# Kernel optimization log

Hardware: AMD Instinct MI355X
Metric: run time of the kernel (lower is better)

Reference implementation:

```python
import jax, jax.numpy as jnp
import numpy as np

B, DV, W, H = 128, 2048, 14, 14
S = W * H            # 196 spatial positions
DQ = 2048            # question vector dim
DA = 1200            # attention dim_v == dim_q == dim_mm (MLB elementwise fusion)
G = 4                # nb_glimpses
DH = 2048            # fusion dim_h (total); per-glimpse = DH // G
NANS = 3000


def setup_inputs() -> dict:
    key = jax.random.key(0)
    ks = jax.random.split(key, 16)
    s = 0.02
    return {
        "input_v": jax.random.normal(ks[0], (B, DV, W, H), jnp.float32),
        "x_q_vec": jax.random.normal(ks[1], (B, DQ), jnp.float32),
        # conv_v_att: 1x1 conv DV->DA  (expressed as channel matmul)
        "Wv_att": jax.random.normal(ks[2], (DV, DA), jnp.float32) * s,
        "bv_att": jnp.zeros((DA,), jnp.float32),
        # linear_q_att: DQ->DA
        "Wq_att": jax.random.normal(ks[3], (DQ, DA), jnp.float32) * s,
        "bq_att": jnp.zeros((DA,), jnp.float32),
        # conv_att: 1x1 conv DA->G
        "Wa": jax.random.normal(ks[4], (DA, G), jnp.float32) * s,
        "ba": jnp.zeros((G,), jnp.float32),
        # per-glimpse fusion linears DV -> DH//G, stacked over glimpses
        "Wf": jax.random.normal(ks[5], (G, DV, DH // G), jnp.float32) * s,
        "bf": jnp.zeros((G, DH // G), jnp.float32),
        # linear_q_fusion: DQ -> DH
        "Wqf": jax.random.normal(ks[6], (DQ, DH), jnp.float32) * s,
        "bqf": jnp.zeros((DH,), jnp.float32),
        # linear_classif: DH -> NANS
        "Wc": jax.random.normal(ks[7], (DH, NANS), jnp.float32) * s,
        "bc": jnp.zeros((NANS,), jnp.float32),
    }


def reference(input_v, x_q_vec, Wv_att, bv_att, Wq_att, bq_att, Wa, ba,
              Wf, bf, Wqf, bqf, Wc, bc):
    b = input_v.shape[0]
    v_flat = input_v.reshape(b, DV, S)                      # [B, DV, S]

    # --- attention scores ---
    # conv_v_att (1x1) + tanh -> [B, S, DA]
    x_v = jnp.tanh(jnp.einsum('bcs,cd->bsd', v_flat, Wv_att) + bv_att)
    # linear_q_att + tanh -> [B, DA], broadcast over spatial
    x_q = jnp.tanh(x_q_vec @ Wq_att + bq_att)
    # MLB fusion_att: elementwise multiply, then tanh (activation_mm)
    x_att = jnp.tanh(x_v * x_q[:, None, :])                 # [B, S, DA]
    scores = jnp.einsum('bsd,dg->bsg', x_att, Wa) + ba      # [B, S, G]
    att = jax.nn.softmax(scores, axis=1)                    # softmax over spatial

    # --- weighted pooling per glimpse ---
    v_att = jnp.einsum('bsg,bcs->bgc', att, v_flat)         # [B, G, DV]

    # --- fusion of glimpses ---
    xv = jnp.tanh(jnp.einsum('bgc,gch->bgh', v_att, Wf) + bf)  # [B, G, DH/G]
    xv = xv.reshape(b, DH)                                   # concat glimpses
    xq = jnp.tanh(x_q_vec @ Wqf + bqf)                       # [B, DH]
    x = xv * xq                                              # MLB fusion_classif

    # --- classifier ---
    x = jnp.tanh(x)
    return x @ Wc + bc                                       # [B, NANS]
```

## Files before the change

### kernel.cpp

```cpp
#include <hip/hip_runtime.h>
#include <hip/hip_bf16.h>

#define BB   128
#define DV   2048
#define SS   196
#define DQ   2048
#define DA   1200
#define DAP  1280
#define GG   4
#define DH   2048
#define NANS 3000
#define NANSP 3008
#define MROWS (BB*SS)
#define NT   5
#define KSPLIT 8
#define KCHUNK (DV/KSPLIT)
#define NQ   (DAP + DH)

typedef __attribute__((ext_vector_type(8))) short bf16x8;
typedef __attribute__((ext_vector_type(4))) float f32x4;

__device__ __forceinline__ float fast_tanh(float x) {
    float e = __expf(2.0f * x);
    return 1.0f - 2.0f * __builtin_amdgcn_rcpf(e + 1.0f);
}

__device__ __forceinline__ void async_copy16(const void* gsrc, void* ldst) {
    __builtin_amdgcn_global_load_lds(
        (const __attribute__((address_space(1))) void*)gsrc,
        (__attribute__((address_space(3))) void*)ldst, 16, 0, 0);
}

__global__ void pad_misc(const float* __restrict__ bv, const float* __restrict__ Wa,
                         float* __restrict__ bvp, float* __restrict__ wap) {
    int i = blockIdx.x * 256 + threadIdx.x;
    if (i < DAP) bvp[i] = (i < DA) ? bv[i] : 0.f;
    if (i < DAP * GG) {
        int d = i >> 2;
        wap[i] = (d < DA) ? Wa[i] : 0.f;
    }
}

__global__ __launch_bounds__(256) void transpose_v(const float* __restrict__ v,
                                                   __hip_bfloat16* __restrict__ vt) {
    __shared__ float tile[128][65];
    const int b  = blockIdx.z;
    const int c0 = blockIdx.x * 128;
    const int s0 = blockIdx.y * 64;
    const int t  = threadIdx.x;
    const int sl = t & 63;
    const int cr = t >> 6;
    const float* src = v + (size_t)b * DV * SS;
    const int sg = s0 + sl;
    const bool sok = sg < SS;
#pragma unroll
    for (int i = 0; i < 32; ++i) {
        int c = cr + i * 4;
        tile[c][sl] = sok ? src[(size_t)(c0 + c) * SS + sg] : 0.f;
    }
    __syncthreads();
    const int cp = (t & 63) * 2;
#pragma unroll
    for (int i = 0; i < 16; ++i) {
        int s = (t >> 6) + i * 4;
        int sgl = s0 + s;
        if (sgl < SS) {
            __hip_bfloat162 h2;
            h2.x = __float2bfloat16(tile[cp][s]);
            h2.y = __float2bfloat16(tile[cp + 1][s]);
            *(__hip_bfloat162*)(vt + ((size_t)b * SS + sgl) * DV + c0 + cp) = h2;
        }
    }
}

__global__ __launch_bounds__(256) void transpose_w(const float* __restrict__ Wv,
                                                   __hip_bfloat16* __restrict__ wvt) {
    __shared__ float tile[64][65];
    const int d0 = blockIdx.x * 64;
    const int c0 = blockIdx.y * 64;
    const int t  = threadIdx.x;
    const int col  = t & 63;
    const int rowb = t >> 6;
#pragma unroll
    for (int i = 0; i < 16; ++i) {
        int c = rowb + i * 4;
        int d = d0 + col;
        tile[c][col] = (d < DA) ? Wv[(size_t)(c0 + c) * DA + d] : 0.f;
    }
    __syncthreads();
#pragma unroll
    for (int i = 0; i < 16; ++i) {
        int dl = rowb + i * 4;
        wvt[(size_t)(d0 + dl) * DV + c0 + col] = __float2bfloat16(tile[col][dl]);
    }
}

template <int SEL>
__global__ __launch_bounds__(256) void gemm_partial(
    const float* __restrict__ A, int lda,
    const float* __restrict__ Bm, const float* __restrict__ B2,
    float* __restrict__ Cp, int Npad) {
    __shared__ float As[64 * 132];
    __shared__ float Bs[64 * 68];
    const int t     = threadIdx.x;
    const int n0    = blockIdx.x * 64;
    const int kbase = blockIdx.y * KCHUNK;

    const float* Aeff = A;
    const float* Beff;
    int ldb, ncol0, nlim;
    if (SEL == 0) {
        Beff = Bm; ldb = NANS; ncol0 = n0; nlim = NANS;
    } else if (SEL == 1) {
        int gg = n0 >> 9;
        Aeff = A + gg * 2048;
        Beff = Bm + (size_t)gg * 2048 * 512;
        ldb = 512; ncol0 = n0 & 511; nlim = 1 << 30;
    } else {
        if (n0 < DAP) { Beff = Bm; ldb = DA; ncol0 = n0;      nlim = DA; }
        else          { Beff = B2; ldb = DH; ncol0 = n0 - DAP; nlim = 1 << 30; }
    }

    const int tm = (t & 31) * 4;
    const int tn = (t >> 5) * 8;
    float acc[4][8] = {};

    for (int k0 = kbase; k0 < kbase + KCHUNK; k0 += 64) {
        {
            int kk = t & 63, mb = (t >> 6) * 32;
#pragma unroll
            for (int i = 0; i < 32; ++i)
                As[kk * 132 + mb + i] = Aeff[(size_t)(mb + i) * lda + k0 + kk];
        }
        {
            int j = t & 63, kr = t >> 6;
            bool ok = (ncol0 + j) < nlim;
#pragma unroll
            for (int i = 0; i < 16; ++i) {
                int k = kr + i * 4;
                Bs[k * 68 + j] = ok ? Beff[(size_t)(k0 + k) * ldb + ncol0 + j] : 0.f;
            }
        }
        __syncthreads();
#pragma unroll
        for (int kk = 0; kk < 64; ++kk) {
            const float4 av = *(const float4*)(As + kk * 132 + tm);
            const float4 b0 = *(const float4*)(Bs + kk * 68 + tn);
            const float4 b1 = *(const float4*)(Bs + kk * 68 + tn + 4);
            const float am[4] = {av.x, av.y, av.z, av.w};
#pragma unroll
            for (int i = 0; i < 4; ++i) {
                acc[i][0] += am[i] * b0.x; acc[i][1] += am[i] * b0.y;
                acc[i][2] += am[i] * b0.z; acc[i][3] += am[i] * b0.w;
                acc[i][4] += am[i] * b1.x; acc[i][5] += am[i] * b1.y;
                acc[i][6] += am[i] * b1.z; acc[i][7] += am[i] * b1.w;
            }
        }
        __syncthreads();
    }
#pragma unroll
    for (int i = 0; i < 4; ++i) {
        size_t base = ((size_t)blockIdx.y * 128 + tm + i) * Npad + n0 + tn;
        float4 v0 = {acc[i][0], acc[i][1], acc[i][2], acc[i][3]};
        float4 v1 = {acc[i][4], acc[i][5], acc[i][6], acc[i][7]};
        *(float4*)(Cp + base) = v0;
        *(float4*)(Cp + base + 4) = v1;
    }
}

template <int MODE>
__global__ __launch_bounds__(256) void gemm_epilogue(
    const float* __restrict__ Cp, int Npad, int Nreal,
    const float* __restrict__ bias, const float* __restrict__ aux,
    float* __restrict__ out, int ldo) {
    int n = blockIdx.x * 256 + threadIdx.x;
    int m = blockIdx.y;
    if (n >= Npad) return;
    float s = 0.f;
#pragma unroll
    for (int ks = 0; ks < KSPLIT; ++ks)
        s += Cp[((size_t)ks * 128 + m) * Npad + n];
    if (MODE == 0) {
        if (n >= Nreal) return;
        out[(size_t)m * ldo + n] = s + bias[n];
    } else {
        float xv = fast_tanh(s + bias[n]);
        out[(size_t)m * ldo + n] = fast_tanh(xv * aux[(size_t)m * 2048 + n]);
    }
}

__global__ __launch_bounds__(256) void epilogue_q(
    const float* __restrict__ Cp,
    const float* __restrict__ bqa, const float* __restrict__ bqf,
    float* __restrict__ qatt, float* __restrict__ qfus) {
    int n = blockIdx.x * 256 + threadIdx.x;
    int m = blockIdx.y;
    if (n >= NQ) return;
    float s = 0.f;
#pragma unroll
    for (int ks = 0; ks < KSPLIT; ++ks)
        s += Cp[((size_t)ks * 128 + m) * NQ + n];
    if (n < DAP) {
        qatt[(size_t)m * DAP + n] = (n < DA) ? fast_tanh(s + bqa[n]) : 0.f;
    } else {
        int j = n - DAP;
        qfus[(size_t)m * DH + j] = fast_tanh(s + bqf[j]);
    }
}

__global__ __launch_bounds__(512, 2) void big_gemm(
    const __hip_bfloat16* __restrict__ vt,
    const __hip_bfloat16* __restrict__ wt,
    const float* __restrict__ bvp,
    const float* __restrict__ qatt,
    const float* __restrict__ wap,
    float* __restrict__ scores_p) {
    __shared__ __align__(16) char lds[131072];
    __shared__ __align__(16) float wa_s[256 * 4];
    __shared__ float qs[3 * 256];

    const int t    = threadIdx.x;
    const int lane = t & 63;
    const int w    = t >> 6;
    const int wr   = w >> 2;
    const int wc   = w & 3;

    int bid = blockIdx.x;
    int grp = bid / 40, r = bid % 40;
    int mt, nt;
    if (grp < 12) { mt = grp * 8 + (r & 7); nt = r >> 3; }
    else          { mt = 96 + (r & 1);      nt = r >> 1; }
    const int m0 = mt * 256, n0 = nt * 256;
    const int b_lo = m0 / SS;
    const int bs1  = (b_lo + 1) * SS;
    const int bs2  = (b_lo + 2) * SS;

    if (t < 256) *(float4*)(wa_s + t * 4) = *(const float4*)(wap + (n0 + t) * 4);
    {
        int j = t >> 8, c = t & 255;
        int b = b_lo + j;
        qs[t] = (b < BB) ? qatt[(size_t)b * DAP + n0 + c] : 0.f;
        if (t < 256) {
            int b2 = b_lo + 2;
            qs[512 + t] = (b2 < BB) ? qatt[(size_t)b2 * DAP + n0 + t] : 0.f;
        }
    }

    const int srow   = lane >> 3;
    const int schunk = (lane & 7) ^ srow;
    const __hip_bfloat16* aG = vt + (size_t)(m0 + w * 8 + srow) * DV + schunk * 8;
    const __hip_bfloat16* bG = wt + (size_t)(n0 + w * 8 + srow) * DV + schunk * 8;

    auto STAGE = [&](int buf, int kk) {
        char* aL = lds + buf * 65536 + w * 1024;
        char* bL = aL + 32768;
#pragma unroll
        for (int j = 0; j < 4; ++j) {
            async_copy16(aG + (size_t)(j * 64) * DV + kk, aL + j * 8192);
            async_copy16(bG + (size_t)(j * 64) * DV + kk, bL + j * 8192);
        }
    };

    f32x4 acc[8][4];
#pragma unroll
    for (int i = 0; i < 8; ++i)
#pragma unroll
        for (int j = 0; j < 4; ++j) acc[i][j] = (f32x4){0.f, 0.f, 0.f, 0.f};

    STAGE(0, 0);

    for (int kt = 0; kt < 32; ++kt) {
        const int cur = kt & 1;
        __builtin_amdgcn_s_barrier();
        if (kt < 31) {
            STAGE(cur ^ 1, (kt + 1) * 64);
            asm volatile("s_waitcnt vmcnt(8)" ::: "memory");
        } else {
            asm volatile("s_waitcnt vmcnt(0)" ::: "memory");
        }
        __builtin_amdgcn_s_barrier();

        const __hip_bfloat16* As = (const __hip_bfloat16*)(lds + cur * 65536);
        const __hip_bfloat16* Bs = As + 16384;
        bf16x8 a[4], b[4];
#pragma unroll
        for (int ks = 0; ks < 2; ++ks) {
            const int cx = ((ks * 4 + (lane >> 4)) ^ (lane & 7)) * 8;
#pragma unroll
            for (int ni = 0; ni < 4; ++ni)
                b[ni] = *(const bf16x8*)(Bs + (wc * 64 + ni * 16 + (lane & 15)) * 64 + cx);
#pragma unroll
            for (int h = 0; h < 2; ++h) {
#pragma unroll
                for (int q = 0; q < 4; ++q)
                    a[q] = *(const bf16x8*)(As + (wr * 128 + (h * 4 + q) * 16 + (lane & 15)) * 64 + cx);
                __builtin_amdgcn_s_setprio(1);
#pragma unroll
                for (int q = 0; q < 4; ++q)
#pragma unroll
                    for (int ni = 0; ni < 4; ++ni)
                        acc[h * 4 + q][ni] = __builtin_amdgcn_mfma_f32_16x16x32_bf16(
                            a[q], b[ni], acc[h * 4 + q][ni], 0, 0, 0);
                __builtin_amdgcn_s_setprio(0);
            }
        }
    }

    __syncthreads();
    float* sc = (float*)lds;

    const int colb_l = wc * 64 + (lane & 15);
    const int colb_g = n0 + colb_l;
    float bvv[4];
    float4 wv[4];
#pragma unroll
    for (int ni = 0; ni < 4; ++ni) {
        bvv[ni] = bvp[colb_g + ni * 16];
        wv[ni]  = *(const float4*)(wa_s + (colb_l + ni * 16) * 4);
    }
#pragma unroll
    for (int mi = 0; mi < 8; ++mi) {
#pragma unroll
        for (int rr = 0; rr < 4; ++rr) {
            int lrow = wr * 128 + mi * 16 + ((lane >> 4) << 2) + rr;
            int row  = m0 + lrow;
            int qoff = (row >= bs1 ? 256 : 0) + (row >= bs2 ? 256 : 0);
            float p0 = 0.f, p1 = 0.f, p2 = 0.f, p3 = 0.f;
#pragma unroll
            for (int ni = 0; ni < 4; ++ni) {
                float xv = fast_tanh(acc[mi][ni][rr] + bvv[ni]);
                float xa = fast_tanh(xv * qs[qoff + colb_l + ni * 16]);
                p0 += xa * wv[ni].x; p1 += xa * wv[ni].y;
                p2 += xa * wv[ni].z; p3 += xa * wv[ni].w;
            }
#pragma unroll
            for (int mk = 1; mk < 16; mk <<= 1) {
                p0 += __shfl_xor(p0, mk); p1 += __shfl_xor(p1, mk);
                p2 += __shfl_xor(p2, mk); p3 += __shfl_xor(p3, mk);
            }
            if ((lane & 15) == 0)
                *(float4*)(sc + ((size_t)wc * 256 + lrow) * 4) =
                    (float4){p0, p1, p2, p3};
        }
    }
    __syncthreads();
    if (t < 256) {
        float4 s0 = *(float4*)(sc + (0 * 256 + t) * 4);
        float4 s1 = *(float4*)(sc + (1 * 256 + t) * 4);
        float4 s2 = *(float4*)(sc + (2 * 256 + t) * 4);
        float4 s3 = *(float4*)(sc + (3 * 256 + t) * 4);
        float4 s = {s0.x + s1.x + s2.x + s3.x, s0.y + s1.y + s2.y + s3.y,
                    s0.z + s1.z + s2.z + s3.z, s0.w + s1.w + s2.w + s3.w};
        *(float4*)(scores_p + ((size_t)nt * MROWS + m0 + t) * 4) = s;
    }
}

__global__ __launch_bounds__(256) void softmax_pool(
    const float* __restrict__ scores_p,
    const __hip_bfloat16* __restrict__ vt,
    float* __restrict__ vatt) {
    __shared__ __align__(16) float att[SS * GG];
    const int b = blockIdx.y;
    const int t = threadIdx.x;
    if (t < SS) {
        float4 s = {0.f, 0.f, 0.f, 0.f};
#pragma unroll
        for (int ntile = 0; ntile < NT; ++ntile) {
            float4 p = *(const float4*)(scores_p + ((size_t)ntile * MROWS + b * SS + t) * 4);
            s.x += p.x; s.y += p.y; s.z += p.z; s.w += p.w;
        }
        *(float4*)(att + t * 4) = s;
    }
    __syncthreads();
    {
        const int g = t >> 6;
        const int lane = t & 63;
        float mx = -3.0e38f;
        for (int s = lane; s < SS; s += 64) mx = fmaxf(mx, att[s * 4 + g]);
#pragma unroll
        for (int m = 32; m > 0; m >>= 1) mx = fmaxf(mx, __shfl_xor(mx, m));
        float sum = 0.f;
        for (int s = lane; s < SS; s += 64) sum += __expf(att[s * 4 + g] - mx);
#pragma unroll
        for (int m = 32; m > 0; m >>= 1) sum += __shfl_xor(sum, m);
        float inv = __builtin_amdgcn_rcpf(sum);
        for (int s = lane; s < SS; s += 64) att[s * 4 + g] = __expf(att[s * 4 + g] - mx) * inv;
    }
    __syncthreads();
    const int c = blockIdx.x * 512 + t * 2;
    const __hip_bfloat16* vp = vt + (size_t)b * SS * DV + c;
    float a00 = 0, a01 = 0, a02 = 0, a03 = 0;
    float a10 = 0, a11 = 0, a12 = 0, a13 = 0;
#pragma unroll 4
    for (int s = 0; s < SS; ++s) {
        unsigned u = *(const unsigned*)(vp + (size_t)s * DV);
        float v0 = __uint_as_float(u << 16);
        float v1 = __uint_as_float(u & 0xffff0000u);
        float4 aw = *(const float4*)(att + s * 4);
        a00 += v0 * aw.x; a01 += v0 * aw.y; a02 += v0 * aw.z; a03 += v0 * aw.w;
        a10 += v1 * aw.x; a11 += v1 * aw.y; a12 += v1 * aw.z; a13 += v1 * aw.w;
    }
    float* vb = vatt + (size_t)b * GG * DV;
    vb[0 * DV + c] = a00; vb[0 * DV + c + 1] = a10;
    vb[1 * DV + c] = a01; vb[1 * DV + c + 1] = a11;
    vb[2 * DV + c] = a02; vb[2 * DV + c + 1] = a12;
    vb[3 * DV + c] = a03; vb[3 * DV + c + 1] = a13;
}

extern "C" void kernel_launch(void* const* d_in, const int* in_sizes, int n_in,
                              void* d_out, int out_size, void* d_ws, size_t ws_size,
                              hipStream_t stream) {
    const float* input_v = (const float*)d_in[0];
    const float* x_q     = (const float*)d_in[1];
    const float* Wv      = (const float*)d_in[2];
    const float* bv      = (const float*)d_in[3];
    const float* Wq_att  = (const float*)d_in[4];
    const float* bq_att  = (const float*)d_in[5];
    const float* Wa      = (const float*)d_in[6];
    const float* Wf      = (const float*)d_in[8];
    const float* bf_     = (const float*)d_in[9];
    const float* Wqf     = (const float*)d_in[10];
    const float* bqf     = (const float*)d_in[11];
    const float* Wc      = (const float*)d_in[12];
    const float* bc      = (const float*)d_in[13];
    float* out = (float*)d_out;

    char* wsb = (char*)d_ws;
    size_t off = 0;
    auto carve = [&](size_t bytes) -> void* {
        void* p = wsb + off;
        off += (bytes + 255) & ~(size_t)255;
        return p;
    };
    __hip_bfloat16* vt  = (__hip_bfloat16*)carve((size_t)MROWS * DV * 2);
    __hip_bfloat16* wvt = (__hip_bfloat16*)carve((size_t)DAP * DV * 2);
    float* Cp       = (float*)carve((size_t)KSPLIT * 128 * NQ * 4);
    float* scores_p = (float*)carve((size_t)NT * MROWS * GG * 4);
    float* qatt = (float*)carve((size_t)BB * DAP * 4);
    float* qfus = (float*)carve((size_t)BB * DH * 4);
    float* bvp  = (float*)carve((size_t)DAP * 4);
    float* wap  = (float*)carve((size_t)DAP * GG * 4);
    float* vatt = (float*)carve((size_t)BB * GG * DV * 4);
    float* xbuf = (float*)carve((size_t)BB * DH * 4);
    (void)ws_size; (void)n_in; (void)in_sizes; (void)out_size;

    pad_misc<<<dim3(20), 256, 0, stream>>>(bv, Wa, bvp, wap);
    transpose_v<<<dim3(DV / 128, 4, BB), 256, 0, stream>>>(input_v, vt);
    transpose_w<<<dim3(DAP / 64, DV / 64), 256, 0, stream>>>(Wv, wvt);

    gemm_partial<2><<<dim3(NQ / 64, KSPLIT), 256, 0, stream>>>(
        x_q, DQ, Wq_att, Wqf, Cp, NQ);
    epilogue_q<<<dim3(NQ / 256, BB), 256, 0, stream>>>(Cp, bq_att, bqf, qatt, qfus);

    big_gemm<<<dim3(490), 512, 0, stream>>>(vt, wvt, bvp, qatt, wap, scores_p);

    softmax_pool<<<dim3(4, BB), 256, 0, stream>>>(scores_p, vt, vatt);

    gemm_partial<1><<<dim3(DH / 64, KSPLIT), 256, 0, stream>>>(
        vatt, GG * DV, Wf, nullptr, Cp, DH);
    gemm_epilogue<2><<<dim3(DH / 256, BB), 256, 0, stream>>>(
        Cp, DH, DH, bf_, qfus, xbuf, DH);

    gemm_partial<0><<<dim3(NANSP / 64, KSPLIT), 256, 0, stream>>>(
        xbuf, DH, Wc, nullptr, Cp, NANSP);
    gemm_epilogue<0><<<dim3(NANSP / 256 + 1, BB), 256, 0, stream>>>(
        Cp, NANSP, NANS, bc, nullptr, out, NANS);
}
```

Before: 764.4 us.

## Interleave async staging with MFMA phases in big GEMM and simplify v transpose

The main GEMM's K-loop is restructured into four sub-phases. Each phase issues part of the next tile's async global-to-LDS loads, waits on a partial vmcnt, and runs its MFMA block between barriers. This spreads memory traffic across the compute and changes the LDS layout and swizzle to split by k-half. The input transpose drops the LDS tile: each thread reads 16 channels strided by S and writes two 16-byte bf16 vectors, trading coalesced reads for simpler code. The extra barriers per iteration could add sync overhead.

```diff
diff --git a/kernel.cpp b/kernel.cpp
--- a/kernel.cpp
+++ b/kernel.cpp
@@ -43,34 +43,23 @@
 
 __global__ __launch_bounds__(256) void transpose_v(const float* __restrict__ v,
                                                    __hip_bfloat16* __restrict__ vt) {
-    __shared__ float tile[128][65];
     const int b  = blockIdx.z;
-    const int c0 = blockIdx.x * 128;
-    const int s0 = blockIdx.y * 64;
-    const int t  = threadIdx.x;
-    const int sl = t & 63;
-    const int cr = t >> 6;
-    const float* src = v + (size_t)b * DV * SS;
-    const int sg = s0 + sl;
-    const bool sok = sg < SS;
-#pragma unroll
-    for (int i = 0; i < 32; ++i) {
-        int c = cr + i * 4;
-        tile[c][sl] = sok ? src[(size_t)(c0 + c) * SS + sg] : 0.f;
-    }
-    __syncthreads();
-    const int cp = (t & 63) * 2;
-#pragma unroll
-    for (int i = 0; i < 16; ++i) {
-        int s = (t >> 6) + i * 4;
-        int sgl = s0 + s;
-        if (sgl < SS) {
-            __hip_bfloat162 h2;
-            h2.x = __float2bfloat16(tile[cp][s]);
-            h2.y = __float2bfloat16(tile[cp + 1][s]);
-            *(__hip_bfloat162*)(vt + ((size_t)b * SS + sgl) * DV + c0 + cp) = h2;
-        }
-    }
+    const int c0 = blockIdx.x * 64 + (threadIdx.x >> 6) * 16;
+    const int s  = blockIdx.y * 64 + (threadIdx.x & 63);
+    if (s >= SS) return;
+    const float* src = v + (size_t)b * DV * SS + (size_t)c0 * SS + s;
+    float f[16];
+#pragma unroll
+    for (int i = 0; i < 16; ++i) f[i] = src[(size_t)i * SS];
+    union { bf16x8 v8; __hip_bfloat16 h[8]; } u0, u1;
+#pragma unroll
+    for (int i = 0; i < 8; ++i) {
+        u0.h[i] = __float2bfloat16(f[i]);
+        u1.h[i] = __float2bfloat16(f[8 + i]);
+    }
+    __hip_bfloat16* dst = vt + ((size_t)b * SS + s) * DV + c0;
+    *(bf16x8*)dst = u0.v8;
+    *(bf16x8*)(dst + 8) = u1.v8;
 }
 
 __global__ __launch_bounds__(256) void transpose_w(const float* __restrict__ Wv,
@@ -245,64 +234,70 @@
             qs[512 + t] = (b2 < BB) ? qatt[(size_t)b2 * DAP + n0 + t] : 0.f;
         }
     }
-
-    const int srow   = lane >> 3;
-    const int schunk = (lane & 7) ^ srow;
-    const __hip_bfloat16* aG = vt + (size_t)(m0 + w * 8 + srow) * DV + schunk * 8;
-    const __hip_bfloat16* bG = wt + (size_t)(n0 + w * 8 + srow) * DV + schunk * 8;
-
-    auto STAGE = [&](int buf, int kk) {
-        char* aL = lds + buf * 65536 + w * 1024;
-        char* bL = aL + 32768;
-#pragma unroll
-        for (int j = 0; j < 4; ++j) {
-            async_copy16(aG + (size_t)(j * 64) * DV + kk, aL + j * 8192);
-            async_copy16(bG + (size_t)(j * 64) * DV + kk, bL + j * 8192);
-        }
+    __syncthreads();
+
+    const int srow   = t >> 2;
+    const int schunk = (t & 3) ^ ((t >> 3) & 3);
+    const __hip_bfloat16* aG = vt + (size_t)(m0 + srow) * DV + schunk * 8;
+    const __hip_bfloat16* bG = wt + (size_t)(n0 + srow) * DV + schunk * 8;
+
+    auto STAGE_ITEM = [&](int buf, int k, int p) {
+        const int ks = p >> 1, mat = p & 1;
+        const __hip_bfloat16* g = (mat ? bG : aG) + (size_t)k * 64 + ks * 32;
+        char* dst = lds + buf * 65536 + ks * 32768 + mat * 16384 + t * 16;
+        async_copy16(g, dst);
+        async_copy16(g + (size_t)128 * DV, dst + 8192);
     };
 
+    const int rchk = ((lane >> 4) ^ (((lane & 15) >> 1) & 3)) * 16;
+    const int aRow = (wr * 128 + (lane & 15)) * 64;
+    const int bRow = (wc * 64 + (lane & 15)) * 64;
+
     f32x4 acc[8][4];
 #pragma unroll
     for (int i = 0; i < 8; ++i)
 #pragma unroll
         for (int j = 0; j < 4; ++j) acc[i][j] = (f32x4){0.f, 0.f, 0.f, 0.f};
 
-    STAGE(0, 0);
+    STAGE_ITEM(0, 0, 0); STAGE_ITEM(0, 0, 1);
+    STAGE_ITEM(0, 0, 2); STAGE_ITEM(0, 0, 3);
+    asm volatile("s_waitcnt vmcnt(4)" ::: "memory");
+    __builtin_amdgcn_s_barrier();
 
     for (int kt = 0; kt < 32; ++kt) {
         const int cur = kt & 1;
-        __builtin_amdgcn_s_barrier();
-        if (kt < 31) {
-            STAGE(cur ^ 1, (kt + 1) * 64);
-            asm volatile("s_waitcnt vmcnt(8)" ::: "memory");
-        } else {
-            asm volatile("s_waitcnt vmcnt(0)" ::: "memory");
-        }
-        __builtin_amdgcn_s_barrier();
-
-        const __hip_bfloat16* As = (const __hip_bfloat16*)(lds + cur * 65536);
-        const __hip_bfloat16* Bs = As + 16384;
-        bf16x8 a[4], b[4];
-#pragma unroll
-        for (int ks = 0; ks < 2; ++ks) {
-            const int cx = ((ks * 4 + (lane >> 4)) ^ (lane & 7)) * 8;
-#pragma unroll
-            for (int ni = 0; ni < 4; ++ni)
-                b[ni] = *(const bf16x8*)(Bs + (wc * 64 + ni * 16 + (lane & 15)) * 64 + cx);
-#pragma unroll
-            for (int h = 0; h < 2; ++h) {
-#pragma unroll
-                for (int q = 0; q < 4; ++q)
-                    a[q] = *(const bf16x8*)(As + (wr * 128 + (h * 4 + q) * 16 + (lane & 15)) * 64 + cx);
-                __builtin_amdgcn_s_setprio(1);
-#pragma unroll
-                for (int q = 0; q < 4; ++q)
-#pragma unroll
-                    for (int ni = 0; ni < 4; ++ni)
-                        acc[h * 4 + q][ni] = __builtin_amdgcn_mfma_f32_16x16x32_bf16(
-                            a[q], b[ni], acc[h * 4 + q][ni], 0, 0, 0);
-                __builtin_amdgcn_s_setprio(0);
-            }
+        const char* Xb = lds + cur * 65536;
+        bf16x8 bfr[4];
+#pragma unroll
+        for (int p = 0; p < 4; ++p) {
+            const int ks = p >> 1, mh = p & 1;
+            const char* Ar = Xb + ks * 32768;
+            bf16x8 afr[4];
+#pragma unroll
+            for (int q = 0; q < 4; ++q)
+                afr[q] = *(const bf16x8*)(Ar + aRow + (mh * 64 + q * 16) * 64 + rchk);
+            if (mh == 0) {
+#pragma unroll
+                for (int ni = 0; ni < 4; ++ni)
+                    bfr[ni] = *(const bf16x8*)(Ar + 16384 + bRow + (ni * 16) * 64 + rchk);
+            }
+            if (kt < 31) STAGE_ITEM(cur ^ 1, kt + 1, p);
+            if (p == 1) {
+                if (kt < 31) asm volatile("s_waitcnt vmcnt(4)" ::: "memory");
+                else         asm volatile("s_waitcnt vmcnt(0)" ::: "memory");
+            } else if (p == 3 && kt < 31) {
+                asm volatile("s_waitcnt vmcnt(4)" ::: "memory");
+            }
+            __builtin_amdgcn_s_barrier();
+            __builtin_amdgcn_s_setprio(1);
+#pragma unroll
+            for (int q = 0; q < 4; ++q)
+#pragma unroll
+                for (int ni = 0; ni < 4; ++ni)
+                    acc[mh * 4 + q][ni] = __builtin_amdgcn_mfma_f32_16x16x32_bf16(
+                        afr[q], bfr[ni], acc[mh * 4 + q][ni], 0, 0, 0);
+            __builtin_amdgcn_s_setprio(0);
+            __builtin_amdgcn_s_barrier();
         }
     }
 
@@ -445,7 +440,7 @@
     (void)ws_size; (void)n_in; (void)in_sizes; (void)out_size;
 
     pad_misc<<<dim3(20), 256, 0, stream>>>(bv, Wa, bvp, wap);
-    transpose_v<<<dim3(DV / 128, 4, BB), 256, 0, stream>>>(input_v, vt);
+    transpose_v<<<dim3(DV / 64, 4, BB), 256, 0, stream>>>(input_v, vt);
     transpose_w<<<dim3(DAP / 64, DV / 64), 256, 0, stream>>>(Wv, wvt);
 
     gemm_partial<2><<<dim3(NQ / 64, KSPLIT), 256, 0, stream>>>(
```

Measured after the change: 677.7 us. 1.13x faster.
